# Optimization experiments

Hardware: AMD Instinct MI355X
Metric: run time of the kernel (lower is better)

Reference implementation:

```python
import jax, jax.numpy as jnp
import numpy as np

B, D, N = 131072, 512, 101
BIG = 1e9
NORM_EPS = 0.1  # F.normalize eps


def setup_inputs() -> dict:
    key = jax.random.key(0)
    k1, k2, k3 = jax.random.split(key, 3)
    embeddings = jax.random.normal(k1, (B, D), dtype=jnp.float32)
    centers_weight = jax.random.normal(k2, (N, D), dtype=jnp.float32)
    labels = jax.random.randint(k3, (B,), 0, N, dtype=jnp.int64)
    return {"embeddings": embeddings, "centers_weight": centers_weight, "labels": labels}


def reference(embeddings, centers_weight, labels):
    # ---- center (MSE) term: per-sample squared distance to own center ----
    gathered = centers_weight[labels]                     # [B, D]
    center_loss = ((embeddings - gathered) ** 2).sum(axis=1)  # [B] (reduction=None)

    # ---- margin term (original operates on .data -> detached) ----
    W = jax.lax.stop_gradient(centers_weight)
    norms = jnp.sqrt((W * W).sum(axis=1, keepdims=True))
    C = W / jnp.maximum(norms, NORM_EPS)                  # F.normalize(p=2, eps=0.1)
    n = C.shape[0]
    dist = 1.0 - C @ C.T                                  # [N, N] cosine distance
    idx = jnp.arange(n)
    diff = jnp.abs(idx[:, None] - idx[None, :])
    dist = dist + BIG * (diff == 0)                       # mask diagonal (eye)

    # neighbor distances BEFORE they are masked out
    d_lower = jnp.diagonal(dist, offset=-1)               # Dist[i, i-1], i = 1..n-1
    d_upper = jnp.diagonal(dist, offset=1)                # Dist[i, i+1], i = 0..n-2

    dist_masked = dist + BIG * (diff == 1)                # mask adjacent centers
    min_dist = dist_masked.min(axis=1)                    # Dist[i, NegIdx]

    margin = (jax.nn.relu(2.0 * d_lower - min_dist[1:]).sum()
              + jax.nn.relu(2.0 * d_upper - min_dist[:-1]).sum()) / n

    return margin + center_loss.mean()
```

## Files before the change

### kernel.cpp

```cpp
#include <hip/hip_runtime.h>

#define BB 131072
#define DD 512
#define NN 101
#define D4 128
#define TOT (BB * D4)
#define CBLK 1024
#define STR (CBLK * 256)
#define NITER 64
#define NWAVE (CBLK * 4)
#define NPAIR (NN * NN)

typedef float f4 __attribute__((ext_vector_type(4)));

__global__ __launch_bounds__(256, 4) void fused_kernel(
    const f4* __restrict__ emb, const f4* __restrict__ ctr,
    const int* __restrict__ labels,
    float* __restrict__ partial,
    float* __restrict__ G)
{
    int b    = blockIdx.x;
    int lane = threadIdx.x & 63;
    int wid  = threadIdx.x >> 6;

    int w = b * 4 + wid;
#pragma unroll
    for (int rep = 0; rep < 3; rep++) {
        int p = w + rep * NWAVE;
        if (p < NPAIR) {
            int i = p / NN;
            int j = p % NN;
            const f4* wi = ctr + i * D4;
            const f4* wj = ctr + j * D4;
            float dot = 0.f;
#pragma unroll
            for (int r = 0; r < 2; r++) {
                f4 a = wi[lane + r * 64];
                f4 c = wj[lane + r * 64];
                dot += a.x * c.x + a.y * c.y + a.z * c.z + a.w * c.w;
            }
            for (int off = 32; off > 0; off >>= 1)
                dot += __shfl_down(dot, off);
            if (lane == 0) G[p] = dot;
        }
    }

    int tid = b * 256 + threadIdx.x;
    int d4  = tid & (D4 - 1);
    float local = 0.f;
#pragma unroll 1
    for (int kk = 0; kk < NITER / 4; kk++) {
        int i0 = tid + (kk * 4 + 0) * STR;
        int i1 = tid + (kk * 4 + 1) * STR;
        int i2 = tid + (kk * 4 + 2) * STR;
        int i3 = tid + (kk * 4 + 3) * STR;
        int l0 = labels[i0 >> 7];
        int l1 = labels[i1 >> 7];
        int l2 = labels[i2 >> 7];
        int l3 = labels[i3 >> 7];
        f4 e0 = __builtin_nontemporal_load(emb + i0);
        f4 e1 = __builtin_nontemporal_load(emb + i1);
        f4 e2 = __builtin_nontemporal_load(emb + i2);
        f4 e3 = __builtin_nontemporal_load(emb + i3);
        f4 c0 = ctr[l0 * D4 + d4];
        f4 c1 = ctr[l1 * D4 + d4];
        f4 c2 = ctr[l2 * D4 + d4];
        f4 c3 = ctr[l3 * D4 + d4];
        f4 t0 = e0 - c0;
        f4 t1 = e1 - c1;
        f4 t2 = e2 - c2;
        f4 t3 = e3 - c3;
        local += t0.x * t0.x + t0.y * t0.y + t0.z * t0.z + t0.w * t0.w;
        local += t1.x * t1.x + t1.y * t1.y + t1.z * t1.z + t1.w * t1.w;
        local += t2.x * t2.x + t2.y * t2.y + t2.z * t2.z + t2.w * t2.w;
        local += t3.x * t3.x + t3.y * t3.y + t3.z * t3.z + t3.w * t3.w;
    }
    for (int off = 32; off > 0; off >>= 1)
        local += __shfl_down(local, off);
    __shared__ float wsum[4];
    if (lane == 0) wsum[wid] = local;
    __syncthreads();
    if (threadIdx.x == 0)
        partial[b] = wsum[0] + wsum[1] + wsum[2] + wsum[3];
}

__global__ __launch_bounds__(256) void finalize_kernel(
    const float* __restrict__ G, const float* __restrict__ partial,
    float* __restrict__ out)
{
    int t = threadIdx.x;

    double dsum = 0.0;
    for (int i = t; i < CBLK; i += 256)
        dsum += (double)partial[i];
    for (int off = 32; off > 0; off >>= 1)
        dsum += __shfl_down(dsum, off);
    __shared__ double dacc[4];
    if ((t & 63) == 0) dacc[t >> 6] = dsum;

    __shared__ float denom[NN];
    __shared__ float mind[NN];
    if (t < NN)
        denom[t] = fmaxf(sqrtf(G[t * NN + t]), 0.1f);
    __syncthreads();
    if (t < NN) {
        float di = denom[t];
        float mn = 1e30f;
        for (int j = 0; j < NN; j++) {
            if (j >= t - 1 && j <= t + 1) continue;
            float d = 1.0f - G[t * NN + j] / (di * denom[j]);
            mn = fminf(mn, d);
        }
        mind[t] = mn;
    }
    __syncthreads();
    float contrib = 0.f;
    if (t >= 1 && t < NN) {
        float dl = 1.0f - G[t * NN + (t - 1)] / (denom[t] * denom[t - 1]);
        contrib += fmaxf(2.0f * dl - mind[t], 0.0f);
    }
    if (t < NN - 1) {
        float du = 1.0f - G[t * NN + (t + 1)] / (denom[t] * denom[t + 1]);
        contrib += fmaxf(2.0f * du - mind[t], 0.0f);
    }
    for (int off = 32; off > 0; off >>= 1)
        contrib += __shfl_down(contrib, off);
    __shared__ float wsum2[4];
    if ((t & 63) == 0) wsum2[t >> 6] = contrib;
    __syncthreads();
    if (t == 0) {
        float margin = (wsum2[0] + wsum2[1] + wsum2[2] + wsum2[3]) / (float)NN;
        double center = (dacc[0] + dacc[1] + dacc[2] + dacc[3]) / (double)BB;
        out[0] = margin + (float)center;
    }
}

extern "C" void kernel_launch(void* const* d_in, const int* in_sizes, int n_in,
                              void* d_out, int out_size, void* d_ws, size_t ws_size,
                              hipStream_t stream) {
    const float* emb    = (const float*)d_in[0];
    const float* ctr    = (const float*)d_in[1];
    const int*   labels = (const int*)d_in[2];
    float* out = (float*)d_out;

    float* partial = (float*)d_ws;
    float* G       = (float*)((char*)d_ws + CBLK * 4);

    fused_kernel<<<CBLK, 256, 0, stream>>>(
        (const f4*)emb, (const f4*)ctr, labels, partial, G);
    finalize_kernel<<<1, 256, 0, stream>>>(G, partial, out);
}
```

Baseline: 82.66 us.

## Stage half of the centers in LDS and split feature dim across blocks

The fused kernel now launches 256 blocks of 1024 threads. Each block loads one half of the center matrix's feature dimension (101x256 floats) into shared memory, along with its 1024 labels. Center gathers and the Gram-matrix dot products then read LDS instead of global/L2, and the Gram matrix is computed as two half-D partials that finalize sums. The cost is about 100KB of LDS per block, so only one block fits per CU. With 256 blocks, per-block staging cost and lower parallelism may limit how well the embedding stream is overlapped.

After: 80.54 us. -2.6%, faster.

```diff
diff --git a/kernel.cpp b/kernel.cpp
--- a/kernel.cpp
+++ b/kernel.cpp
@@ -4,68 +4,77 @@
 #define DD 512
 #define NN 101
 #define D4 128
-#define TOT (BB * D4)
-#define CBLK 1024
-#define STR (CBLK * 256)
-#define NITER 64
-#define NWAVE (CBLK * 4)
+#define HALF 64
+#define NBLK 256
+#define BTHR 1024
+#define SPB 1024
 #define NPAIR (NN * NN)
+#define PPB 80
 
 typedef float f4 __attribute__((ext_vector_type(4)));
 
-__global__ __launch_bounds__(256, 4) void fused_kernel(
+__global__ __launch_bounds__(BTHR, 1) void fused_kernel(
     const f4* __restrict__ emb, const f4* __restrict__ ctr,
     const int* __restrict__ labels,
     float* __restrict__ partial,
-    float* __restrict__ G)
+    float* __restrict__ G0,
+    float* __restrict__ G1)
 {
+    __shared__ f4  sctr[NN * HALF];
+    __shared__ int slab[SPB];
+    __shared__ float wsum[16];
+
     int b    = blockIdx.x;
-    int lane = threadIdx.x & 63;
-    int wid  = threadIdx.x >> 6;
+    int h    = b >> 7;
+    int blk  = b & 127;
+    int tid  = threadIdx.x;
+    int wid  = tid >> 6;
+    int lane = tid & 63;
 
-    int w = b * 4 + wid;
+    for (int idx = tid; idx < NN * HALF; idx += BTHR) {
+        int row = idx >> 6;
+        int c   = idx & 63;
+        sctr[idx] = ctr[row * D4 + h * HALF + c];
+    }
+    slab[tid] = labels[blk * SPB + tid];
+    __syncthreads();
+
+    float* Gh = h ? G1 : G0;
 #pragma unroll
-    for (int rep = 0; rep < 3; rep++) {
-        int p = w + rep * NWAVE;
+    for (int rep = 0; rep < 5; rep++) {
+        int p = blk * PPB + rep * 16 + wid;
         if (p < NPAIR) {
             int i = p / NN;
             int j = p % NN;
-            const f4* wi = ctr + i * D4;
-            const f4* wj = ctr + j * D4;
-            float dot = 0.f;
-#pragma unroll
-            for (int r = 0; r < 2; r++) {
-                f4 a = wi[lane + r * 64];
-                f4 c = wj[lane + r * 64];
-                dot += a.x * c.x + a.y * c.y + a.z * c.z + a.w * c.w;
-            }
+            f4 a = sctr[i * HALF + lane];
+            f4 c = sctr[j * HALF + lane];
+            float dot = a.x * c.x + a.y * c.y + a.z * c.z + a.w * c.w;
             for (int off = 32; off > 0; off >>= 1)
                 dot += __shfl_down(dot, off);
-            if (lane == 0) G[p] = dot;
+            if (lane == 0) Gh[p] = dot;
         }
     }
 
-    int tid = b * 256 + threadIdx.x;
-    int d4  = tid & (D4 - 1);
     float local = 0.f;
 #pragma unroll 1
-    for (int kk = 0; kk < NITER / 4; kk++) {
-        int i0 = tid + (kk * 4 + 0) * STR;
-        int i1 = tid + (kk * 4 + 1) * STR;
-        int i2 = tid + (kk * 4 + 2) * STR;
-        int i3 = tid + (kk * 4 + 3) * STR;
-        int l0 = labels[i0 >> 7];
-        int l1 = labels[i1 >> 7];
-        int l2 = labels[i2 >> 7];
-        int l3 = labels[i3 >> 7];
-        f4 e0 = __builtin_nontemporal_load(emb + i0);
-        f4 e1 = __builtin_nontemporal_load(emb + i1);
-        f4 e2 = __builtin_nontemporal_load(emb + i2);
-        f4 e3 = __builtin_nontemporal_load(emb + i3);
-        f4 c0 = ctr[l0 * D4 + d4];
-        f4 c1 = ctr[l1 * D4 + d4];
-        f4 c2 = ctr[l2 * D4 + d4];
-        f4 c3 = ctr[l3 * D4 + d4];
+    for (int kk = 0; kk < 16; kk++) {
+        int q0 = (kk * 4 + 0) * 16 + wid;
+        int q1 = (kk * 4 + 1) * 16 + wid;
+        int q2 = (kk * 4 + 2) * 16 + wid;
+        int q3 = (kk * 4 + 3) * 16 + wid;
+        int l0 = slab[q0];
+        int l1 = slab[q1];
+        int l2 = slab[q2];
+        int l3 = slab[q3];
+        const f4* base = emb + h * HALF + lane;
+        f4 e0 = __builtin_nontemporal_load(base + (blk * SPB + q0) * D4);
+        f4 e1 = __builtin_nontemporal_load(base + (blk * SPB + q1) * D4);
+        f4 e2 = __builtin_nontemporal_load(base + (blk * SPB + q2) * D4);
+        f4 e3 = __builtin_nontemporal_load(base + (blk * SPB + q3) * D4);
+        f4 c0 = sctr[l0 * HALF + lane];
+        f4 c1 = sctr[l1 * HALF + lane];
+        f4 c2 = sctr[l2 * HALF + lane];
+        f4 c3 = sctr[l3 * HALF + lane];
         f4 t0 = e0 - c0;
         f4 t1 = e1 - c1;
         f4 t2 = e2 - c2;
@@ -77,22 +86,23 @@
     }
     for (int off = 32; off > 0; off >>= 1)
         local += __shfl_down(local, off);
-    __shared__ float wsum[4];
     if (lane == 0) wsum[wid] = local;
     __syncthreads();
-    if (threadIdx.x == 0)
-        partial[b] = wsum[0] + wsum[1] + wsum[2] + wsum[3];
+    if (tid == 0) {
+        float s = 0.f;
+#pragma unroll
+        for (int w = 0; w < 16; w++) s += wsum[w];
+        partial[b] = s;
+    }
 }
 
 __global__ __launch_bounds__(256) void finalize_kernel(
-    const float* __restrict__ G, const float* __restrict__ partial,
-    float* __restrict__ out)
+    const float* __restrict__ G0, const float* __restrict__ G1,
+    const float* __restrict__ partial, float* __restrict__ out)
 {
     int t = threadIdx.x;
 
-    double dsum = 0.0;
-    for (int i = t; i < CBLK; i += 256)
-        dsum += (double)partial[i];
+    double dsum = (t < NBLK) ? (double)partial[t] : 0.0;
     for (int off = 32; off > 0; off >>= 1)
         dsum += __shfl_down(dsum, off);
     __shared__ double dacc[4];
@@ -101,14 +111,15 @@
     __shared__ float denom[NN];
     __shared__ float mind[NN];
     if (t < NN)
-        denom[t] = fmaxf(sqrtf(G[t * NN + t]), 0.1f);
+        denom[t] = fmaxf(sqrtf(G0[t * NN + t] + G1[t * NN + t]), 0.1f);
     __syncthreads();
     if (t < NN) {
         float di = denom[t];
         float mn = 1e30f;
         for (int j = 0; j < NN; j++) {
             if (j >= t - 1 && j <= t + 1) continue;
-            float d = 1.0f - G[t * NN + j] / (di * denom[j]);
+            float g = G0[t * NN + j] + G1[t * NN + j];
+            float d = 1.0f - g / (di * denom[j]);
             mn = fminf(mn, d);
         }
         mind[t] = mn;
@@ -116,11 +127,13 @@
     __syncthreads();
     float contrib = 0.f;
     if (t >= 1 && t < NN) {
-        float dl = 1.0f - G[t * NN + (t - 1)] / (denom[t] * denom[t - 1]);
+        float g = G0[t * NN + (t - 1)] + G1[t * NN + (t - 1)];
+        float dl = 1.0f - g / (denom[t] * denom[t - 1]);
         contrib += fmaxf(2.0f * dl - mind[t], 0.0f);
     }
     if (t < NN - 1) {
-        float du = 1.0f - G[t * NN + (t + 1)] / (denom[t] * denom[t + 1]);
+        float g = G0[t * NN + (t + 1)] + G1[t * NN + (t + 1)];
+        float du = 1.0f - g / (denom[t] * denom[t + 1]);
         contrib += fmaxf(2.0f * du - mind[t], 0.0f);
     }
     for (int off = 32; off > 0; off >>= 1)
@@ -144,9 +157,10 @@
     float* out = (float*)d_out;
 
     float* partial = (float*)d_ws;
-    float* G       = (float*)((char*)d_ws + CBLK * 4);
+    float* G0      = (float*)((char*)d_ws + 1024);
+    float* G1      = G0 + NPAIR;
 
-    fused_kernel<<<CBLK, 256, 0, stream>>>(
-        (const f4*)emb, (const f4*)ctr, labels, partial, G);
-    finalize_kernel<<<1, 256, 0, stream>>>(G, partial, out);
+    fused_kernel<<<NBLK, BTHR, 0, stream>>>(
+        (const f4*)emb, (const f4*)ctr, labels, partial, G0, G1);
+    finalize_kernel<<<1, 256, 0, stream>>>(G0, G1, partial, out);
 }
```
